# Optimization experiments

Measured on AMD Instinct MI355X. Metric: run time of the kernel, lower is better.

The kernel has to match this reference:

```python
import jax, jax.numpy as jnp
import numpy as np

EMBED = 1024
KEY = 64
HEAD = 64
CTX = 4096
BATCH = 8


def _linear(x, w, b):
    # torch nn.Linear: y = x @ W.T + b, W shape [out, in]
    return x @ w.T + b


def setup_inputs() -> dict:
    key = jax.random.key(0)
    ks = jax.random.split(key, 11)
    s_e = 1.0 / np.sqrt(EMBED)
    s_k = 1.0 / np.sqrt(KEY)
    return {
        "embeddings": jax.random.normal(ks[0], (BATCH, CTX, EMBED), dtype=jnp.float32),
        "kw1": jax.random.uniform(ks[1], (KEY, EMBED), jnp.float32, -s_e, s_e),
        "kb1": jax.random.uniform(ks[2], (KEY,), jnp.float32, -s_e, s_e),
        "kw2": jax.random.uniform(ks[3], (KEY, KEY), jnp.float32, -s_k, s_k),
        "kb2": jax.random.uniform(ks[4], (KEY,), jnp.float32, -s_k, s_k),
        "qw1": jax.random.uniform(ks[5], (KEY, EMBED), jnp.float32, -s_e, s_e),
        "qb1": jax.random.uniform(ks[6], (KEY,), jnp.float32, -s_e, s_e),
        "qw2": jax.random.uniform(ks[7], (KEY, KEY), jnp.float32, -s_k, s_k),
        "qb2": jax.random.uniform(ks[8], (KEY,), jnp.float32, -s_k, s_k),
        "vw": jax.random.uniform(ks[9], (HEAD, EMBED), jnp.float32, -s_e, s_e),
        "vb": jax.random.uniform(ks[10], (HEAD,), jnp.float32, -s_e, s_e),
    }


def reference(embeddings, kw1, kb1, kw2, kb2, qw1, qb1, qw2, qb2, vw, vb):
    T = embeddings.shape[1]
    keys = jax.nn.relu(_linear(jax.nn.relu(_linear(embeddings, kw1, kb1)), kw2, kb2))
    queries = jax.nn.relu(_linear(jax.nn.relu(_linear(embeddings, qw1, qb1)), qw2, qb2))
    values = _linear(embeddings, vw, vb)
    # scores: [B, T, T]
    scores = jnp.einsum("btk,bsk->bts", queries, keys) / np.sqrt(KEY).astype(np.float32)
    # Faithful to original: tril(ones) * -1e10 added (masks lower triangle incl. diagonal)
    mask = jnp.tril(jnp.ones((T, T), dtype=jnp.float32)) * jnp.float32(-1e10)
    weights = jax.nn.softmax(scores + mask, axis=-1)
    return jnp.einsum("bts,bsh->bth", weights, values)
```

## Files before the change

kernel.cpp:

```cpp
#include <hip/hip_runtime.h>
#include <hip/hip_bf16.h>
#include <math.h>

#define NB   8
#define TCTX 4096
#define ED   1024
#define KD   64

typedef __attribute__((ext_vector_type(8))) short bf16x8;
typedef __attribute__((ext_vector_type(4))) float f32x4;

#define LOG2E  1.44269504088896340736f
#define SCALE2 (0.125f * LOG2E)
#define MASK2  (-1e10f * LOG2E)

__device__ __forceinline__ void lds_fence() {
    asm volatile("s_waitcnt lgkmcnt(0)" ::: "memory");
    __builtin_amdgcn_sched_barrier(0);
}

__device__ __forceinline__ unsigned short f2bf(float f) {
    union { float f; unsigned u; } c; c.f = f;
    return (unsigned short)((c.u + 0x7FFFu + ((c.u >> 16) & 1u)) >> 16);
}
__device__ __forceinline__ int swz(int row, int byteoff) {
    return row * 128 + (byteoff ^ ((row & 7) << 4));
}
__device__ __forceinline__ f32x4 fzero4() {
    f32x4 z; z[0] = 0.f; z[1] = 0.f; z[2] = 0.f; z[3] = 0.f; return z;
}
__device__ __forceinline__ void gl_lds16(const void* g, void* l) {
    __builtin_amdgcn_global_load_lds(
        (const __attribute__((address_space(1))) unsigned int*)g,
        (__attribute__((address_space(3))) unsigned int*)l, 16, 0, 0);
}
__device__ __forceinline__ unsigned cvtpk_bf16(float lo, float hi) {
    unsigned r;
    asm("v_cvt_pk_bf16_f32 %0, %1, %2" : "=v"(r) : "v"(lo), "v"(hi));
    return r;
}

__global__ __launch_bounds__(256) void prep_kernel(
    const float* __restrict__ kw1, const float* __restrict__ qw1,
    const float* __restrict__ vw,  const float* __restrict__ kw2,
    const float* __restrict__ qw2,
    unsigned short* __restrict__ W1p, unsigned short* __restrict__ W2p)
{
    int idx = blockIdx.x * 256 + threadIdx.x;
    if (idx < 24576) {
        int ks = idx / 1536, rem = idx % 1536;
        int r = rem >> 3, bb = rem & 7;
        int c = bb ^ (r & 7);
        const float* src = (r < 64)  ? (kw1 + r * ED)
                         : (r < 128) ? (qw1 + (r - 64) * ED)
                                     : (vw  + (r - 128) * ED);
        src += ks * 64 + c * 8;
        unsigned short* dst = W1p + (size_t)idx * 8;
        #pragma unroll
        for (int e = 0; e < 8; ++e) dst[e] = f2bf(src[e]);
    } else if (idx < 25600) {
        int j = idx - 24576;
        int lane = j & 63, kh = (j >> 6) & 1, n = (j >> 7) & 3, kq = j >> 9;
        int row = n * 16 + (lane & 15);
        int ko  = kh * 32 + (lane >> 4) * 8;
        const float* src = (kq ? qw2 : kw2) + row * 64 + ko;
        unsigned short* dst = W2p + (size_t)j * 8;
        #pragma unroll
        for (int e = 0; e < 8; ++e) dst[e] = f2bf(src[e]);
    }
}

__global__ __launch_bounds__(256, 2) void proj_kernel(
    const float* __restrict__ emb,
    const unsigned short* __restrict__ W1p, const unsigned short* __restrict__ W2p,
    const float* __restrict__ kb1, const float* __restrict__ kb2,
    const float* __restrict__ qb1, const float* __restrict__ qb2,
    const float* __restrict__ vb,
    unsigned short* __restrict__ Qo, unsigned short* __restrict__ Ko,
    unsigned short* __restrict__ Vt)
{
    __shared__ __align__(16) char lds[80 * 1024];

    const int tid  = threadIdx.x;
    const int lane = tid & 63;
    const int w    = tid >> 6;
    const int lr   = lane & 15;
    const int lg   = lane >> 4;
    const long r0  = (long)blockIdx.x * 64;
    const int  b   = blockIdx.x >> 6;
    const int  tb  = (blockIdx.x & 63) * 64;

    const float* embB = emb + r0 * ED;

    f32x4 acc[12];
    #pragma unroll
    for (int j = 0; j < 12; ++j) acc[j] = fzero4();

    auto stageA = [&](int buf, int ks) {
        char* Abuf = lds + buf * 16 * 1024;
        const float* eb = embB + ks * 64;
        #pragma unroll
        for (int j = 0; j < 4; ++j) {
            int chunk = j * 4 + w;
            int r = chunk * 4 + (lane >> 4);
            int c = (lane & 15) ^ (r & 7);
            gl_lds16(eb + (long)r * ED + c * 4, Abuf + chunk * 1024);
        }
    };
    auto stageB = [&](int buf, int ks) {
        char* Bbuf = lds + 32 * 1024 + buf * 24 * 1024;
        const unsigned short* wb = W1p + (size_t)ks * 12288;
        #pragma unroll
        for (int j = 0; j < 6; ++j) {
            int chunk = j * 4 + w;
            gl_lds16(wb + chunk * 512 + lane * 8, Bbuf + chunk * 1024);
        }
    };

    stageA(0, 0); stageB(0, 0);
    __syncthreads();

    int cur = 0;
    for (int ks = 0; ks < 16; ++ks) {
        if (ks < 15) { stageA(cur ^ 1, ks + 1); stageB(cur ^ 1, ks + 1); }
        char* Ac = lds + cur * 16 * 1024;
        char* Bc = lds + 32 * 1024 + cur * 24 * 1024;
        const int r = w * 16 + lr;
        #pragma unroll
        for (int kh = 0; kh < 2; ++kh) {
            int cb0 = kh * 8 + lg * 2;
            float4 fa = *(const float4*)(Ac + r * 256 + ((cb0 ^ (r & 7)) * 16));
            float4 fb = *(const float4*)(Ac + r * 256 + (((cb0 + 1) ^ (r & 7)) * 16));
            bf16x8 a;
            a[0] = (short)f2bf(fa.x); a[1] = (short)f2bf(fa.y);
            a[2] = (short)f2bf(fa.z); a[3] = (short)f2bf(fa.w);
            a[4] = (short)f2bf(fb.x); a[5] = (short)f2bf(fb.y);
            a[6] = (short)f2bf(fb.z); a[7] = (short)f2bf(fb.w);
            #pragma unroll
            for (int n = 0; n < 12; ++n) {
                bf16x8 bv = *(const bf16x8*)(Bc + swz(n * 16 + lr, kh * 64 + lg * 16));
                acc[n] = __builtin_amdgcn_mfma_f32_16x16x32_bf16(a, bv, acc[n], 0, 0, 0);
            }
        }
        __syncthreads();
        cur ^= 1;
    }

    char* H  = lds + w * 2048;
    char* VT = lds + 16 * 1024;

    #pragma unroll
    for (int kq = 0; kq < 2; ++kq) {
        const float* b1 = kq ? qb1 : kb1;
        const float* b2 = kq ? qb2 : kb2;
        unsigned short* dst = kq ? Qo : Ko;
        const float oscale = kq ? SCALE2 : 1.0f;
        #pragma unroll
        for (int n = 0; n < 4; ++n) {
            int col = n * 16 + lr;
            float bias = b1[col];
            #pragma unroll
            for (int rr = 0; rr < 4; ++rr) {
                int row = lg * 4 + rr;
                *(unsigned short*)(H + swz(row, col * 2)) =
                    f2bf(fmaxf(acc[kq * 4 + n][rr] + bias, 0.f));
            }
        }
        lds_fence();
        bf16x8 a2k0 = *(const bf16x8*)(H + swz(lr, 0 * 64 + lg * 16));
        bf16x8 a2k1 = *(const bf16x8*)(H + swz(lr, 1 * 64 + lg * 16));
        lds_fence();

        f32x4 acc2[4];
        #pragma unroll
        for (int n = 0; n < 4; ++n) acc2[n] = fzero4();
        #pragma unroll
        for (int n = 0; n < 4; ++n) {
            bf16x8 w2f0 = *(const bf16x8*)(W2p + ((kq * 4 + n) * 2 + 0) * 512 + lane * 8);
            bf16x8 w2f1 = *(const bf16x8*)(W2p + ((kq * 4 + n) * 2 + 1) * 512 + lane * 8);
            acc2[n] = __builtin_amdgcn_mfma_f32_16x16x32_bf16(a2k0, w2f0, acc2[n], 0, 0, 0);
            acc2[n] = __builtin_amdgcn_mfma_f32_16x16x32_bf16(a2k1, w2f1, acc2[n], 0, 0, 0);
        }
        #pragma unroll
        for (int n = 0; n < 4; ++n) {
            int col = n * 16 + lr;
            float bias = b2[col];
            #pragma unroll
            for (int rr = 0; rr < 4; ++rr) {
                long rg = r0 + w * 16 + lg * 4 + rr;
                dst[rg * KD + col] = f2bf(fmaxf(acc2[n][rr] + bias, 0.f) * oscale);
            }
        }
    }

    #pragma unroll
    for (int n = 0; n < 4; ++n) {
        int col = n * 16 + lr;
        float bias = vb[col];
        #pragma unroll
        for (int rr = 0; rr < 4; ++rr) {
            int tl = w * 16 + lg * 4 + rr;
            *(unsigned short*)(VT + swz(col, tl * 2)) = f2bf(acc[8 + n][rr] + bias);
        }
    }
    __syncthreads();
    #pragma unroll
    for (int it = 0; it < 2; ++it) {
        int c = it * 256 + tid;
        int h = c >> 3, c4 = c & 7;
        *(int4*)(Vt + ((long)b * KD + h) * TCTX + tb + c4 * 8) =
            *(const int4*)(VT + swz(h, c4 * 16));
    }
}

__global__ __launch_bounds__(128) void attn_kernel(
    const unsigned short* __restrict__ Qb,
    const unsigned short* __restrict__ Kb,
    const unsigned short* __restrict__ Vt,
    float* __restrict__ Opart, float2* __restrict__ MSum)
{
    __shared__ __align__(16) char lds[24 * 1024];

    const int bid  = blockIdx.x;
    const int b    = bid & 7;
    const int half = (bid >> 3) & 1;
    const int qr   = bid >> 4;
    const int qi   = (qr + 127) & 127;
    const int t0   = qi * 32;
    const int tid = threadIdx.x, lane = tid & 63, w = tid >> 6;
    const int lr  = lane & 15, lg = lane >> 4;
    const int tg  = t0 + w * 16 + lr;

    const unsigned short* Qg  = Qb + ((long)b * TCTX + t0 + w * 16) * KD;
    const unsigned short* Kg0 = Kb + (long)b * TCTX * KD;
    const unsigned short* Vg0 = Vt + (long)b * KD * TCTX;

    const int srow = lane >> 3;
    const int sblk = lane & 7;

    const int s0q = (qi == 127) ? 0 : (qi >> 1);
    const int len = 64 - s0q;
    const int mid = s0q + ((len + 1) >> 1);
    const int s_lo = half ? mid : s0q;
    const int s_hi = half ? 64  : mid;

    auto stageK = [&](int si) {
        const unsigned short* Kg = Kg0 + si * 64 * KD;
        #pragma unroll
        for (int j = 0; j < 4; ++j) {
            int chunk = w * 4 + j;
            int r = chunk * 8 + srow;
            int c = sblk ^ (r & 7);
            gl_lds16(Kg + r * KD + c * 8, lds + chunk * 1024);
        }
    };
    auto stageV = [&](int buf, int si) {
        char* Vl = lds + 8 * 1024 + buf * 8 * 1024;
        const unsigned short* Vg = Vg0 + si * 64;
        #pragma unroll
        for (int j = 0; j < 4; ++j) {
            int chunk = w * 4 + j;
            int r = chunk * 8 + srow;
            int c = sblk ^ (r & 7);
            gl_lds16(Vg + (long)r * TCTX + c * 8, Vl + chunk * 1024);
        }
    };

    float m2 = MASK2, sum_p = 0.f;
    f32x4 O[4];
    #pragma unroll
    for (int n = 0; n < 4; ++n) O[n] = fzero4();

    if (s_lo < s_hi) {
        char* QP = lds + 16 * 1024 + w * 2048;
        #pragma unroll
        for (int j = 0; j < 2; ++j) {
            int r = j * 8 + srow;
            int c = sblk ^ (r & 7);
            gl_lds16(Qg + r * KD + c * 8, QP + j * 1024);
        }
        stageK(s_lo);
        stageV(0, s_lo);
        __syncthreads();

        bf16x8 qf[2];
        #pragma unroll
        for (int kh = 0; kh < 2; ++kh)
            qf[kh] = *(const bf16x8*)(QP + swz(lr, kh * 64 + lg * 16));

        int cur = 0;
        for (int si = s_lo; si < s_hi; ++si) {
            f32x4 sc[4];
            #pragma unroll
            for (int mi = 0; mi < 4; ++mi) sc[mi] = fzero4();
            __builtin_amdgcn_s_setprio(1);
            #pragma unroll
            for (int kh = 0; kh < 2; ++kh) {
                #pragma unroll
                for (int mi = 0; mi < 4; ++mi) {
                    bf16x8 kf = *(const bf16x8*)(lds + swz(mi * 16 + lr, kh * 64 + lg * 16));
                    sc[mi] = __builtin_amdgcn_mfma_f32_16x16x32_bf16(kf, qf[kh], sc[mi], 0, 0, 0);
                }
            }
            __builtin_amdgcn_s_setprio(0);

            __syncthreads();
            if (si + 1 < s_hi) {
                stageK(si + 1);
                stageV(cur ^ 1, si + 1);
            }

            const int thr = tg - si * 64;
            float s2v[4][4];
            #pragma unroll
            for (int mi = 0; mi < 4; ++mi)
                #pragma unroll
                for (int rr = 0; rr < 4; ++rr) {
                    int sl = mi * 16 + lg * 4 + rr;
                    s2v[mi][rr] = (sl <= thr) ? MASK2 : sc[mi][rr];
                }

            float pml = s2v[0][0];
            #pragma unroll
            for (int mi = 0; mi < 4; ++mi)
                #pragma unroll
                for (int rr = 0; rr < 4; ++rr) pml = fmaxf(pml, s2v[mi][rr]);

            if (!__all(pml - m2 <= 8.0f)) {
                float pm = pml;
                pm = fmaxf(pm, __shfl_xor(pm, 16, 64));
                pm = fmaxf(pm, __shfl_xor(pm, 32, 64));
                float mnew = fmaxf(m2, pm);
                float scl = __builtin_amdgcn_exp2f(m2 - mnew);
                m2 = mnew;
                sum_p *= scl;
                #pragma unroll
                for (int rr = 0; rr < 4; ++rr) {
                    float sb = __shfl(scl, lg * 4 + rr, 64);
                    #pragma unroll
                    for (int n = 0; n < 4; ++n) O[n][rr] *= sb;
                }
            }
            float ls = 0.f;
            #pragma unroll
            for (int mi = 0; mi < 4; ++mi)
                #pragma unroll
                for (int rr = 0; rr < 4; ++rr) {
                    s2v[mi][rr] = __builtin_amdgcn_exp2f(s2v[mi][rr] - m2);
                    ls += s2v[mi][rr];
                }
            sum_p += ls;

            unsigned W[4][2];
            #pragma unroll
            for (int mi = 0; mi < 4; ++mi) {
                W[mi][0] = cvtpk_bf16(s2v[mi][0], s2v[mi][1]);
                W[mi][1] = cvtpk_bf16(s2v[mi][2], s2v[mi][3]);
            }
            const int lgh  = lg >> 1;
            const int bsrc = 2 * (lg & 1);
            union { unsigned u[4]; bf16x8 v; } apu0, apu1;
            #pragma unroll
            for (int jj = 0; jj < 4; ++jj) {
                int srcl = ((bsrc + (jj >> 1)) << 4) | lr;
                unsigned lo0 = __shfl(W[0][jj & 1], srcl, 64);
                unsigned hi0 = __shfl(W[1][jj & 1], srcl, 64);
                unsigned lo1 = __shfl(W[2][jj & 1], srcl, 64);
                unsigned hi1 = __shfl(W[3][jj & 1], srcl, 64);
                apu0.u[jj] = lgh ? hi0 : lo0;
                apu1.u[jj] = lgh ? hi1 : lo1;
            }

            char* Vl = lds + 8 * 1024 + cur * 8 * 1024;
            __builtin_amdgcn_s_setprio(1);
            #pragma unroll
            for (int n = 0; n < 4; ++n) {
                bf16x8 bv0 = *(const bf16x8*)(Vl + swz(n * 16 + lr, 0 * 64 + lg * 16));
                bf16x8 bv1 = *(const bf16x8*)(Vl + swz(n * 16 + lr, 1 * 64 + lg * 16));
                O[n] = __builtin_amdgcn_mfma_f32_16x16x32_bf16(apu0.v, bv0, O[n], 0, 0, 0);
                O[n] = __builtin_amdgcn_mfma_f32_16x16x32_bf16(apu1.v, bv1, O[n], 0, 0, 0);
            }
            __builtin_amdgcn_s_setprio(0);

            __syncthreads();
            cur ^= 1;
        }
    }

    float sr = sum_p;
    sr += __shfl_xor(sr, 16, 64);
    sr += __shfl_xor(sr, 32, 64);
    const long rbase = (long)b * TCTX + t0 + w * 16;
    #pragma unroll
    for (int rr = 0; rr < 4; ++rr) {
        int tl = lg * 4 + rr;
        long rowi = (rbase + tl) * 2 + half;
        #pragma unroll
        for (int n = 0; n < 4; ++n)
            Opart[rowi * 64 + n * 16 + lr] = O[n][rr];
    }
    if (lg == 0)
        MSum[(rbase + lr) * 2 + half] = make_float2(m2, sr);
}

__global__ __launch_bounds__(256) void combine_kernel(
    const float* __restrict__ Opart, const float2* __restrict__ MSum,
    float* __restrict__ out)
{
    const long total = (long)NB * TCTX * KD;
    for (long idx = (long)blockIdx.x * 256 + threadIdx.x; idx < total;
         idx += (long)gridDim.x * 256) {
        long r = idx >> 6;
        int  h = (int)(idx & 63);
        float2 A = MSum[r * 2 + 0];
        float2 B = MSum[r * 2 + 1];
        float M  = fmaxf(A.x, B.x);
        float wa = __builtin_amdgcn_exp2f(A.x - M);
        float wb = __builtin_amdgcn_exp2f(B.x - M);
        float denom = A.y * wa + B.y * wb;
        float oa = Opart[(r * 2 + 0) * 64 + h];
        float ob = Opart[(r * 2 + 1) * 64 + h];
        out[idx] = (oa * wa + ob * wb) / denom;
    }
}

extern "C" void kernel_launch(void* const* d_in, const int* in_sizes, int n_in,
                              void* d_out, int out_size, void* d_ws, size_t ws_size,
                              hipStream_t stream) {
    const float* emb = (const float*)d_in[0];
    const float* kw1 = (const float*)d_in[1];
    const float* kb1 = (const float*)d_in[2];
    const float* kw2 = (const float*)d_in[3];
    const float* kb2 = (const float*)d_in[4];
    const float* qw1 = (const float*)d_in[5];
    const float* qb1 = (const float*)d_in[6];
    const float* qw2 = (const float*)d_in[7];
    const float* qb2 = (const float*)d_in[8];
    const float* vw  = (const float*)d_in[9];
    const float* vb  = (const float*)d_in[10];

    unsigned short* Qb  = (unsigned short*)d_ws;
    unsigned short* Kb  = Qb + (size_t)NB * TCTX * KD;
    unsigned short* Vt  = Kb + (size_t)NB * TCTX * KD;
    unsigned short* W1p = Vt + (size_t)NB * TCTX * KD;
    unsigned short* W2p = W1p + 196608;
    float*  Opart = (float*)(W2p + 8192);
    float2* MSum  = (float2*)(Opart + (size_t)NB * TCTX * 2 * KD);

    hipLaunchKernelGGL(prep_kernel, dim3(100), dim3(256), 0, stream,
                       kw1, qw1, vw, kw2, qw2, W1p, W2p);
    hipLaunchKernelGGL(proj_kernel, dim3(512), dim3(256), 0, stream,
                       emb, W1p, W2p, kb1, kb2, qb1, qb2, vb,
                       Qb, Kb, Vt);
    hipLaunchKernelGGL(attn_kernel, dim3(2048), dim3(128), 0, stream,
                       Qb, Kb, Vt, Opart, MSum);
    hipLaunchKernelGGL(combine_kernel, dim3(2048), dim3(256), 0, stream,
                       Opart, MSum, (float*)d_out);
}
```

Before: 91.46 us.

## Drop V double buffer and Q LDS staging to cut LDS and raise occupancy

The attention kernel's LDS shrinks from 24KB to 16KB by removing the second V buffer and loading Q fragments straight from global into registers. V for the next tile is now staged after the PV MFMAs finish, and launch_bounds asks for 5 blocks per CU. The goal is more resident blocks to hide latency. In exchange, V loads for the next iteration are no longer overlapped with the softmax and PV work of the current one, so each iteration waits on V at the next barrier.

```diff
diff --git a/kernel.cpp b/kernel.cpp
--- a/kernel.cpp
+++ b/kernel.cpp
@@ -213,13 +213,13 @@
     }
 }
 
-__global__ __launch_bounds__(128) void attn_kernel(
+__global__ __launch_bounds__(128, 5) void attn_kernel(
     const unsigned short* __restrict__ Qb,
     const unsigned short* __restrict__ Kb,
     const unsigned short* __restrict__ Vt,
     float* __restrict__ Opart, float2* __restrict__ MSum)
 {
-    __shared__ __align__(16) char lds[24 * 1024];
+    __shared__ __align__(16) char lds[16 * 1024];
 
     const int bid  = blockIdx.x;
     const int b    = bid & 7;
@@ -231,6 +231,9 @@
     const int lr  = lane & 15, lg = lane >> 4;
     const int tg  = t0 + w * 16 + lr;
 
+    char* Kl = lds;
+    char* Vl = lds + 8 * 1024;
+
     const unsigned short* Qg  = Qb + ((long)b * TCTX + t0 + w * 16) * KD;
     const unsigned short* Kg0 = Kb + (long)b * TCTX * KD;
     const unsigned short* Vg0 = Vt + (long)b * KD * TCTX;
@@ -251,11 +254,10 @@
             int chunk = w * 4 + j;
             int r = chunk * 8 + srow;
             int c = sblk ^ (r & 7);
-            gl_lds16(Kg + r * KD + c * 8, lds + chunk * 1024);
+            gl_lds16(Kg + r * KD + c * 8, Kl + chunk * 1024);
         }
     };
-    auto stageV = [&](int buf, int si) {
-        char* Vl = lds + 8 * 1024 + buf * 8 * 1024;
+    auto stageV = [&](int si) {
         const unsigned short* Vg = Vg0 + si * 64;
         #pragma unroll
         for (int j = 0; j < 4; ++j) {
@@ -272,23 +274,14 @@
     for (int n = 0; n < 4; ++n) O[n] = fzero4();
 
     if (s_lo < s_hi) {
-        char* QP = lds + 16 * 1024 + w * 2048;
-        #pragma unroll
-        for (int j = 0; j < 2; ++j) {
-            int r = j * 8 + srow;
-            int c = sblk ^ (r & 7);
-            gl_lds16(Qg + r * KD + c * 8, QP + j * 1024);
-        }
+        bf16x8 qf[2];
+        #pragma unroll
+        for (int kh = 0; kh < 2; ++kh)
+            qf[kh] = *(const bf16x8*)(Qg + lr * KD + kh * 32 + lg * 8);
         stageK(s_lo);
-        stageV(0, s_lo);
+        stageV(s_lo);
         __syncthreads();
 
-        bf16x8 qf[2];
-        #pragma unroll
-        for (int kh = 0; kh < 2; ++kh)
-            qf[kh] = *(const bf16x8*)(QP + swz(lr, kh * 64 + lg * 16));
-
-        int cur = 0;
         for (int si = s_lo; si < s_hi; ++si) {
             f32x4 sc[4];
             #pragma unroll
@@ -298,17 +291,14 @@
             for (int kh = 0; kh < 2; ++kh) {
                 #pragma unroll
                 for (int mi = 0; mi < 4; ++mi) {
-                    bf16x8 kf = *(const bf16x8*)(lds + swz(mi * 16 + lr, kh * 64 + lg * 16));
+                    bf16x8 kf = *(const bf16x8*)(Kl + swz(mi * 16 + lr, kh * 64 + lg * 16));
                     sc[mi] = __builtin_amdgcn_mfma_f32_16x16x32_bf16(kf, qf[kh], sc[mi], 0, 0, 0);
                 }
             }
             __builtin_amdgcn_s_setprio(0);
 
             __syncthreads();
-            if (si + 1 < s_hi) {
-                stageK(si + 1);
-                stageV(cur ^ 1, si + 1);
-            }
+            if (si + 1 < s_hi) stageK(si + 1);
 
             const int thr = tg - si * 64;
             float s2v[4][4];
@@ -371,7 +361,6 @@
                 apu1.u[jj] = lgh ? hi1 : lo1;
             }
 
-            char* Vl = lds + 8 * 1024 + cur * 8 * 1024;
             __builtin_amdgcn_s_setprio(1);
             #pragma unroll
             for (int n = 0; n < 4; ++n) {
@@ -383,7 +372,7 @@
             __builtin_amdgcn_s_setprio(0);
 
             __syncthreads();
-            cur ^= 1;
+            if (si + 1 < s_hi) stageV(si + 1);
         }
     }
 
```

New measurement: 94.74 us. 3.6% more time.
